# Performance work log

Measured on AMD Instinct MI355X. Metric: run time of the kernel, lower is better.

Reference implementation:

```python
import jax, jax.numpy as jnp
import numpy as np

B, N, DIM = 16, 1024, 512
H, DH = 8, 64  # heads, dim_head; inner_dim = H*DH = 512
MASK_VAL = -1e-9  # value ASSIGNED (not added) to diagonal, per original code


def setup_inputs() -> dict:
    key = jax.random.key(0)
    ks = jax.random.split(key, 8)
    w = 0.02  # small init so softmax is not saturated
    x = jax.random.normal(ks[0], (B, N, DIM), dtype=jnp.float32)
    Wq = jax.random.normal(ks[1], (DIM, H * DH), dtype=jnp.float32) * w
    Wkv = jax.random.normal(ks[2], (DIM, 2 * H * DH), dtype=jnp.float32) * w
    scale = jnp.full((H,), DH ** -0.5, dtype=jnp.float32)  # nn.Parameter(scale*ones(heads))
    mix_pre = jax.random.normal(ks[3], (H, H), dtype=jnp.float32) * w
    mix_post = jax.random.normal(ks[4], (H, H), dtype=jnp.float32) * w
    Wout = jax.random.normal(ks[5], (H * DH, DIM), dtype=jnp.float32) * w
    bout = jnp.zeros((DIM,), dtype=jnp.float32)
    return {"x": x, "Wq": Wq, "Wkv": Wkv, "scale": scale,
            "mix_pre": mix_pre, "mix_post": mix_post, "Wout": Wout, "bout": bout}


def reference(x, Wq, Wkv, scale, mix_pre, mix_post, Wout, bout):
    b, n, _ = x.shape
    # projections -> [b, h, n, d]
    q = (x @ Wq).reshape(b, n, H, DH).transpose(0, 2, 1, 3)
    kv = (x @ Wkv).reshape(b, n, 2, H, DH)
    k = kv[:, :, 0].transpose(0, 2, 1, 3)
    v = kv[:, :, 1].transpose(0, 2, 1, 3)
    # LMSA: per-head learned scale
    dots = jnp.einsum('bhid,bhjd->bhij', q, k) * scale[None, :, None, None]
    # if_patch_attn: set diagonal entries to -1e-9 (assignment, as in torch)
    eye = jnp.eye(n, dtype=bool)
    dots = jnp.where(eye, jnp.float32(MASK_VAL), dots)
    # talking heads: pre-softmax head mix
    dots = jnp.einsum('bhij,hg->bgij', dots, mix_pre)
    attn = jax.nn.softmax(dots, axis=-1)
    # post-softmax head mix
    attn = jnp.einsum('bhij,hg->bgij', attn, mix_post)
    out = jnp.einsum('bhij,bhjd->bhid', attn, v)  # [b,h,n,d]
    out = out.transpose(0, 2, 1, 3).reshape(b, n, H * DH)
    return out @ Wout + bout
```

## Files before the change

kernel.cpp:

```cpp
#include <hip/hip_runtime.h>
#include <math.h>


typedef short bf16x8 __attribute__((ext_vector_type(8)));
typedef float f32x4 __attribute__((ext_vector_type(4)));

__device__ __forceinline__ f32x4 mfma16(bf16x8 a, bf16x8 b, f32x4 c) {
  return __builtin_amdgcn_mfma_f32_16x16x32_bf16(a, b, c, 0, 0, 0);
}

__device__ __forceinline__ unsigned short f2bf(float f) {
  unsigned u = __float_as_uint(f);
  u = (u + 0x7fffu + ((u >> 16) & 1u)) >> 16;
  return (unsigned short)u;
}

__device__ __forceinline__ void splitbf(float f, unsigned short& hi,
                                        unsigned short& lo) {
  hi = f2bf(f);
  float fh = __uint_as_float((unsigned)hi << 16);
  lo = f2bf(f - fh);
}

__device__ __forceinline__ f32x4 zero4() {
  f32x4 z = {0.f, 0.f, 0.f, 0.f};
  return z;
}

namespace {

constexpr int kB = 16, kN = 1024, kH = 8;

__global__ __launch_bounds__(256) void prep(
    const float* __restrict__ Wq, const float* __restrict__ Wkv,
    const float* __restrict__ Wout, unsigned short* __restrict__ WTh,
    unsigned short* __restrict__ WTl, unsigned short* __restrict__ WoTh,
    unsigned short* __restrict__ WoTl) {
  int id = blockIdx.x * 256 + threadIdx.x;
  unsigned short h, l;
  if (id < 1536 * 512) {
    int n = id >> 9, k = id & 511;
    float v = (n < 512) ? Wq[(size_t)k * 512 + n]
                        : Wkv[(size_t)k * 1024 + (n - 512)];
    splitbf(v, h, l);
    WTh[id] = h; WTl[id] = l;
  } else {
    int id2 = id - 1536 * 512;
    int n = id2 >> 9, k = id2 & 511;
    splitbf(Wout[(size_t)k * 512 + n], h, l);
    WoTh[id2] = h; WoTl[id2] = l;
  }
}

__global__ __launch_bounds__(256) void gemm_qkv(
    const float* __restrict__ X, const unsigned short* __restrict__ WTh,
    const unsigned short* __restrict__ WTl, const float* __restrict__ scale,
    unsigned short* __restrict__ Qh, unsigned short* __restrict__ Ql,
    unsigned short* __restrict__ Kh, unsigned short* __restrict__ Kl,
    unsigned short* __restrict__ Vh, unsigned short* __restrict__ Vl) {
  __shared__ unsigned short Ah[128 * 72], Al[128 * 72];
  __shared__ unsigned short Bh[128 * 72], Bl[128 * 72];
  const int tid = threadIdx.x;
  const int n0 = blockIdx.x * 128, m0 = blockIdx.y * 128;
  const int w = tid >> 6, lane = tid & 63, quad = lane >> 4, ln = lane & 15;
  const int mw = (w >> 1) * 64, nw = (w & 1) * 64;
  const int srow = tid >> 3, schk = (tid & 7) * 8;
  f32x4 acc[4][4];
#pragma unroll
  for (int i = 0; i < 4; ++i)
#pragma unroll
    for (int j = 0; j < 4; ++j) acc[i][j] = zero4();
  for (int k0 = 0; k0 < 512; k0 += 64) {
    float xa[4][8];
    uint4 bh4[4], bl4[4];
#pragma unroll
    for (int c2 = 0; c2 < 4; ++c2) {
      const float* xs = X + (size_t)(m0 + c2 * 32 + srow) * 512 + k0 + schk;
      *(float4*)&xa[c2][0] = *(const float4*)xs;
      *(float4*)&xa[c2][4] = *(const float4*)(xs + 4);
      size_t boff = (size_t)(n0 + c2 * 32 + srow) * 512 + k0 + schk;
      bh4[c2] = *(const uint4*)(WTh + boff);
      bl4[c2] = *(const uint4*)(WTl + boff);
    }
    __syncthreads();
#pragma unroll
    for (int c2 = 0; c2 < 4; ++c2) {
      unsigned short hh[8], ll[8];
#pragma unroll
      for (int e = 0; e < 8; ++e) splitbf(xa[c2][e], hh[e], ll[e]);
      uint4 ph, pl;
      ph.x = hh[0] | ((unsigned)hh[1] << 16); pl.x = ll[0] | ((unsigned)ll[1] << 16);
      ph.y = hh[2] | ((unsigned)hh[3] << 16); pl.y = ll[2] | ((unsigned)ll[3] << 16);
      ph.z = hh[4] | ((unsigned)hh[5] << 16); pl.z = ll[4] | ((unsigned)ll[5] << 16);
      ph.w = hh[6] | ((unsigned)hh[7] << 16); pl.w = ll[6] | ((unsigned)ll[7] << 16);
      *(uint4*)&Ah[(c2 * 32 + srow) * 72 + schk] = ph;
      *(uint4*)&Al[(c2 * 32 + srow) * 72 + schk] = pl;
      *(uint4*)&Bh[(c2 * 32 + srow) * 72 + schk] = bh4[c2];
      *(uint4*)&Bl[(c2 * 32 + srow) * 72 + schk] = bl4[c2];
    }
    __syncthreads();
#pragma unroll
    for (int ks = 0; ks < 2; ++ks) {
      bf16x8 afh[4], afl[4], bfh[4], bfl[4];
#pragma unroll
      for (int t = 0; t < 4; ++t) {
        int ao = (mw + t * 16 + ln) * 72 + ks * 32 + quad * 8;
        int bo = (nw + t * 16 + ln) * 72 + ks * 32 + quad * 8;
        afh[t] = *(const bf16x8*)&Ah[ao];
        afl[t] = *(const bf16x8*)&Al[ao];
        bfh[t] = *(const bf16x8*)&Bh[bo];
        bfl[t] = *(const bf16x8*)&Bl[bo];
      }
#pragma unroll
      for (int mt = 0; mt < 4; ++mt)
#pragma unroll
        for (int nt = 0; nt < 4; ++nt) {
          acc[mt][nt] = mfma16(afh[mt], bfh[nt], acc[mt][nt]);
          acc[mt][nt] = mfma16(afh[mt], bfl[nt], acc[mt][nt]);
          acc[mt][nt] = mfma16(afl[mt], bfh[nt], acc[mt][nt]);
        }
    }
  }
  const int region = n0 >> 9;
#pragma unroll
  for (int nt = 0; nt < 4; ++nt) {
    const int col = n0 + nw + nt * 16 + ln;
    const int local = col - region * 512;
    const int hh = local >> 6, d = local & 63;
    const float sc = (region == 0) ? scale[hh] : 1.f;
#pragma unroll
    for (int mt = 0; mt < 4; ++mt) {
#pragma unroll
      for (int r = 0; r < 4; ++r) {
        const int row = m0 + mw + mt * 16 + quad * 4 + r;
        const int b = row >> 10, i = row & 1023;
        unsigned short vh, vl;
        splitbf(acc[mt][nt][r] * sc, vh, vl);
        if (region == 0) {
          size_t o = (((size_t)(b * 8 + hh) * 1024 + i) << 6) + d;
          Qh[o] = vh; Ql[o] = vl;
        } else if (region == 1) {
          size_t o = (((size_t)(b * 8 + hh) * 1024 + i) << 6) + d;
          Kh[o] = vh; Kl[o] = vl;
        } else {
          size_t o = (((size_t)(b * 8 + hh) * 64 + d) << 10) + i;
          Vh[o] = vh; Vl[o] = vl;
        }
      }
    }
  }
}

__global__ __launch_bounds__(256) void attn_lsum(
    const unsigned short* __restrict__ Qh_g, const unsigned short* __restrict__ Ql_g,
    const unsigned short* __restrict__ Kh, const unsigned short* __restrict__ Kl,
    const float* __restrict__ mix_pre, float* __restrict__ IL) {
  __shared__ unsigned short Qsh[128 * 72];
  __shared__ float mixp_s[64], dfix_s[8];
  __shared__ float lred[512];
  const int tid = threadIdx.x;
  const int b = blockIdx.y, ib = blockIdx.x, i0 = ib * 16;
  const int w = tid >> 6, lane = tid & 63, quad = lane >> 4, ln = lane & 15;
  const int jh = w * 16;
  if (tid < 64) mixp_s[tid] = mix_pre[tid];
  if (tid < 8) {
    float s = 0.f;
#pragma unroll
    for (int h = 0; h < 8; ++h) s += mix_pre[h * 8 + tid];
    dfix_s[tid] = -1e-9f * s;
  }
#pragma unroll
  for (int c = 0; c < 4; ++c) {
    int v = tid + 256 * c;
    int row = v >> 3, chk = (v & 7) * 8;
    int h = row >> 4, ii = row & 15;
    *(uint4*)&Qsh[row * 72 + chk] =
        *(const uint4*)(Qh_g + (((size_t)(b * 8 + h) * 1024 + i0 + ii) << 6) + chk);
  }
  __syncthreads();
  const int ig0 = i0 + quad * 4;
  float l[8][4];
#pragma unroll
  for (int a = 0; a < 8; ++a)
#pragma unroll
    for (int r = 0; r < 4; ++r) l[a][r] = 0.f;
  const size_t qoff = (((size_t)(b * 8) * 1024 + i0 + ln) << 6) + quad * 8;
#pragma unroll 1
  for (int j0 = 0; j0 < 1024; j0 += 64) {
    const int jj = j0 + jh + ln;
    bf16x8 kh_r[2][2], kl_r[2][2], ql_r[2][2];
#pragma unroll
    for (int ks = 0; ks < 2; ++ks) {
      size_t kro = (((size_t)(b * 8) * 1024 + jj) << 6) + ks * 32 + quad * 8;
      kh_r[0][ks] = *(const bf16x8*)(Kh + kro);
      kl_r[0][ks] = *(const bf16x8*)(Kl + kro);
      ql_r[0][ks] = *(const bf16x8*)(Ql_g + qoff + ks * 32);
    }
    f32x4 S[8];
    int cur = 0;
#pragma unroll
    for (int h = 0; h < 8; ++h) {
      const int nxt = cur ^ 1;
      if (h < 7) {
#pragma unroll
        for (int ks = 0; ks < 2; ++ks) {
          size_t kro = (((size_t)(b * 8 + h + 1) * 1024 + jj) << 6) + ks * 32 + quad * 8;
          kh_r[nxt][ks] = *(const bf16x8*)(Kh + kro);
          kl_r[nxt][ks] = *(const bf16x8*)(Kl + kro);
          ql_r[nxt][ks] = *(const bf16x8*)(Ql_g + qoff + (size_t)(h + 1) * 65536 + ks * 32);
        }
      }
      f32x4 acc = zero4();
#pragma unroll
      for (int ks = 0; ks < 2; ++ks) {
        bf16x8 ah = *(const bf16x8*)&Qsh[(h * 16 + ln) * 72 + ks * 32 + quad * 8];
        acc = mfma16(ah, kh_r[cur][ks], acc);
        acc = mfma16(ah, kl_r[cur][ks], acc);
        acc = mfma16(ql_r[cur][ks], kh_r[cur][ks], acc);
      }
      S[h] = acc;
      cur = nxt;
    }
    const int dr = jj - ig0;
#pragma unroll
    for (int a = 0; a < 8; ++a) {
      f32x4 sm = S[0] * mixp_s[a];
#pragma unroll
      for (int h = 1; h < 8; ++h) sm += S[h] * mixp_s[h * 8 + a];
      const float df = dfix_s[a];
#pragma unroll
      for (int r = 0; r < 4; ++r) {
        float vv = (r == dr) ? df : sm[r];
        l[a][r] += __expf(vv);
      }
    }
  }
#pragma unroll
  for (int off = 1; off < 16; off <<= 1)
#pragma unroll
    for (int a = 0; a < 8; ++a)
#pragma unroll
      for (int r = 0; r < 4; ++r) l[a][r] += __shfl_xor(l[a][r], off);
  if (ln == 0) {
#pragma unroll
    for (int a = 0; a < 8; ++a)
#pragma unroll
      for (int r = 0; r < 4; ++r)
        lred[(w * 8 + a) * 16 + quad * 4 + r] = l[a][r];
  }
  __syncthreads();
  if (tid < 128) {
    int a = tid >> 4, i = tid & 15;
    float s = lred[a * 16 + i] + lred[(8 + a) * 16 + i] +
              lred[(16 + a) * 16 + i] + lred[(24 + a) * 16 + i];
    IL[(((size_t)b * 8 + a) << 10) + i0 + i] = 1.f / s;
  }
}

__global__ __launch_bounds__(256) void attn_pv(
    const unsigned short* __restrict__ Qh_g, const unsigned short* __restrict__ Ql_g,
    const unsigned short* __restrict__ Kh, const unsigned short* __restrict__ Kl,
    const unsigned short* __restrict__ Vh, const unsigned short* __restrict__ Vl,
    const float* __restrict__ IL, const float* __restrict__ mix_pre,
    const float* __restrict__ mix_post, float* __restrict__ OA) {
  __shared__ unsigned short Qsh[128 * 72];
  __shared__ unsigned short Wsh[128 * 72], Wsl[128 * 72];
  __shared__ float mixp_s[64], mixq_s[64], dfix_s[8];
  __shared__ float Ils[8][16];
  const int tid = threadIdx.x;
  const int b = blockIdx.y, ib = blockIdx.x, i0 = ib * 16;
  const int w = tid >> 6, lane = tid & 63, quad = lane >> 4, ln = lane & 15;
  const int jh = w * 16;
  if (tid < 64) { mixp_s[tid] = mix_pre[tid]; mixq_s[tid] = mix_post[tid]; }
  if (tid < 8) {
    float s = 0.f;
#pragma unroll
    for (int h = 0; h < 8; ++h) s += mix_pre[h * 8 + tid];
    dfix_s[tid] = -1e-9f * s;
  }
  if (tid >= 128) {
    int a = (tid - 128) >> 4, i = tid & 15;
    Ils[a][i] = IL[(((size_t)b * 8 + a) << 10) + i0 + i];
  }
#pragma unroll
  for (int c = 0; c < 4; ++c) {
    int v = tid + 256 * c;
    int row = v >> 3, chk = (v & 7) * 8;
    int h = row >> 4, ii = row & 15;
    *(uint4*)&Qsh[row * 72 + chk] =
        *(const uint4*)(Qh_g + (((size_t)(b * 8 + h) * 1024 + i0 + ii) << 6) + chk);
  }
  __syncthreads();
  const int ig0 = i0 + quad * 4;
  const int cw = w * 2;
  const size_t qoff = (((size_t)(b * 8) * 1024 + i0 + ln) << 6) + quad * 8;
  f32x4 O[2][4];
#pragma unroll
  for (int cc = 0; cc < 2; ++cc)
#pragma unroll
    for (int nt = 0; nt < 4; ++nt) O[cc][nt] = zero4();
  bf16x8 vbh[2][4], vbl[2][4];
#pragma unroll
  for (int nt = 0; nt < 4; ++nt) {
    size_t vo = (((size_t)(b * 8 + cw) * 64 + nt * 16 + ln) << 10) + quad * 8;
    vbh[0][nt] = *(const bf16x8*)(Vh + vo);
    vbl[0][nt] = *(const bf16x8*)(Vl + vo);
  }
#pragma unroll 1
  for (int j0 = 0; j0 < 1024; j0 += 64) {
    const int jj = j0 + jh + ln;
    bf16x8 kh_r[2][2], kl_r[2][2], ql_r[2][2];
#pragma unroll
    for (int ks = 0; ks < 2; ++ks) {
      size_t kro = (((size_t)(b * 8) * 1024 + jj) << 6) + ks * 32 + quad * 8;
      kh_r[0][ks] = *(const bf16x8*)(Kh + kro);
      kl_r[0][ks] = *(const bf16x8*)(Kl + kro);
      ql_r[0][ks] = *(const bf16x8*)(Ql_g + qoff + ks * 32);
    }
    f32x4 S[8];
    int cur = 0;
#pragma unroll
    for (int h = 0; h < 8; ++h) {
      const int nxt = cur ^ 1;
      if (h < 7) {
#pragma unroll
        for (int ks = 0; ks < 2; ++ks) {
          size_t kro = (((size_t)(b * 8 + h + 1) * 1024 + jj) << 6) + ks * 32 + quad * 8;
          kh_r[nxt][ks] = *(const bf16x8*)(Kh + kro);
          kl_r[nxt][ks] = *(const bf16x8*)(Kl + kro);
          ql_r[nxt][ks] = *(const bf16x8*)(Ql_g + qoff + (size_t)(h + 1) * 65536 + ks * 32);
        }
      }
      f32x4 acc = zero4();
#pragma unroll
      for (int ks = 0; ks < 2; ++ks) {
        bf16x8 ah = *(const bf16x8*)&Qsh[(h * 16 + ln) * 72 + ks * 32 + quad * 8];
        acc = mfma16(ah, kh_r[cur][ks], acc);
        acc = mfma16(ah, kl_r[cur][ks], acc);
        acc = mfma16(ql_r[cur][ks], kh_r[cur][ks], acc);
      }
      S[h] = acc;
      cur = nxt;
    }
    const int dr = jj - ig0;
    f32x4 P[8];
#pragma unroll
    for (int a = 0; a < 8; ++a) {
      f32x4 sm = S[0] * mixp_s[a];
#pragma unroll
      for (int h = 1; h < 8; ++h) sm += S[h] * mixp_s[h * 8 + a];
      const float df = dfix_s[a];
      f32x4 il4 = *(const f32x4*)&Ils[a][quad * 4];
      f32x4 p;
#pragma unroll
      for (int r = 0; r < 4; ++r) {
        float vv = (r == dr) ? df : sm[r];
        p[r] = __expf(vv) * il4[r];
      }
      P[a] = p;
    }
#pragma unroll
    for (int c = 0; c < 8; ++c) {
      f32x4 wv = P[0] * mixq_s[c];
#pragma unroll
      for (int a = 1; a < 8; ++a) wv += P[a] * mixq_s[a * 8 + c];
#pragma unroll
      for (int r = 0; r < 4; ++r) {
        unsigned short vhh, vll;
        splitbf(wv[r], vhh, vll);
        int o = (c * 16 + quad * 4 + r) * 72 + jh + ln;
        Wsh[o] = vhh; Wsl[o] = vll;
      }
    }
    __syncthreads();
#pragma unroll
    for (int s = 0; s < 4; ++s) {
      const int cc = s >> 1, ks = s & 1;
      const int c = cw + cc;
      const int vcur = s & 1, vnxt = vcur ^ 1;
      if (s < 3) {
        const int cc2 = (s + 1) >> 1, ks2 = (s + 1) & 1;
#pragma unroll
        for (int nt = 0; nt < 4; ++nt) {
          size_t vo = (((size_t)(b * 8 + cw + cc2) * 64 + nt * 16 + ln) << 10) +
                      j0 + ks2 * 32 + quad * 8;
          vbh[vnxt][nt] = *(const bf16x8*)(Vh + vo);
          vbl[vnxt][nt] = *(const bf16x8*)(Vl + vo);
        }
      } else if (j0 < 960) {
#pragma unroll
        for (int nt = 0; nt < 4; ++nt) {
          size_t vo = (((size_t)(b * 8 + cw) * 64 + nt * 16 + ln) << 10) +
                      j0 + 64 + quad * 8;
          vbh[vnxt][nt] = *(const bf16x8*)(Vh + vo);
          vbl[vnxt][nt] = *(const bf16x8*)(Vl + vo);
        }
      }
      bf16x8 a_h = *(const bf16x8*)&Wsh[(c * 16 + ln) * 72 + ks * 32 + quad * 8];
      bf16x8 a_l = *(const bf16x8*)&Wsl[(c * 16 + ln) * 72 + ks * 32 + quad * 8];
#pragma unroll
      for (int nt = 0; nt < 4; ++nt) {
        O[cc][nt] = mfma16(a_h, vbh[vcur][nt], O[cc][nt]);
        O[cc][nt] = mfma16(a_h, vbl[vcur][nt], O[cc][nt]);
        O[cc][nt] = mfma16(a_l, vbh[vcur][nt], O[cc][nt]);
      }
    }
    __syncthreads();
  }
#pragma unroll
  for (int cc = 0; cc < 2; ++cc)
#pragma unroll
    for (int nt = 0; nt < 4; ++nt)
#pragma unroll
      for (int r = 0; r < 4; ++r) {
        const int i = i0 + quad * 4 + r;
        const int col = (cw + cc) * 64 + nt * 16 + ln;
        OA[((size_t)(b * 1024 + i) << 9) + col] = O[cc][nt][r];
      }
}

__global__ __launch_bounds__(256) void gemm_out(
    const float* __restrict__ A, const unsigned short* __restrict__ BTh,
    const unsigned short* __restrict__ BTl, const float* __restrict__ bias,
    float* __restrict__ Out) {
  __shared__ unsigned short Ah[128 * 72], Al[128 * 72];
  __shared__ unsigned short Bh[128 * 72], Bl[128 * 72];
  const int tid = threadIdx.x;
  const int n0 = blockIdx.x * 128, m0 = blockIdx.y * 128;
  const int w = tid >> 6, lane = tid & 63, quad = lane >> 4, ln = lane & 15;
  const int mw = (w >> 1) * 64, nw = (w & 1) * 64;
  const int srow = tid >> 3, schk = (tid & 7) * 8;
  f32x4 acc[4][4];
#pragma unroll
  for (int i = 0; i < 4; ++i)
#pragma unroll
    for (int j = 0; j < 4; ++j) acc[i][j] = zero4();
  for (int k0 = 0; k0 < 512; k0 += 64) {
    float xa[4][8];
    uint4 bh4[4], bl4[4];
#pragma unroll
    for (int c2 = 0; c2 < 4; ++c2) {
      const float* xs = A + (size_t)(m0 + c2 * 32 + srow) * 512 + k0 + schk;
      *(float4*)&xa[c2][0] = *(const float4*)xs;
      *(float4*)&xa[c2][4] = *(const float4*)(xs + 4);
      size_t boff = (size_t)(n0 + c2 * 32 + srow) * 512 + k0 + schk;
      bh4[c2] = *(const uint4*)(BTh + boff);
      bl4[c2] = *(const uint4*)(BTl + boff);
    }
    __syncthreads();
#pragma unroll
    for (int c2 = 0; c2 < 4; ++c2) {
      unsigned short hh[8], ll[8];
#pragma unroll
      for (int e = 0; e < 8; ++e) splitbf(xa[c2][e], hh[e], ll[e]);
      uint4 ph, pl;
      ph.x = hh[0] | ((unsigned)hh[1] << 16); pl.x = ll[0] | ((unsigned)ll[1] << 16);
      ph.y = hh[2] | ((unsigned)hh[3] << 16); pl.y = ll[2] | ((unsigned)ll[3] << 16);
      ph.z = hh[4] | ((unsigned)hh[5] << 16); pl.z = ll[4] | ((unsigned)ll[5] << 16);
      ph.w = hh[6] | ((unsigned)hh[7] << 16); pl.w = ll[6] | ((unsigned)ll[7] << 16);
      *(uint4*)&Ah[(c2 * 32 + srow) * 72 + schk] = ph;
      *(uint4*)&Al[(c2 * 32 + srow) * 72 + schk] = pl;
      *(uint4*)&Bh[(c2 * 32 + srow) * 72 + schk] = bh4[c2];
      *(uint4*)&Bl[(c2 * 32 + srow) * 72 + schk] = bl4[c2];
    }
    __syncthreads();
#pragma unroll
    for (int ks = 0; ks < 2; ++ks) {
      bf16x8 afh[4], afl[4], bfh[4], bfl[4];
#pragma unroll
      for (int t = 0; t < 4; ++t) {
        int ao = (mw + t * 16 + ln) * 72 + ks * 32 + quad * 8;
        int bo = (nw + t * 16 + ln) * 72 + ks * 32 + quad * 8;
        afh[t] = *(const bf16x8*)&Ah[ao];
        afl[t] = *(const bf16x8*)&Al[ao];
        bfh[t] = *(const bf16x8*)&Bh[bo];
        bfl[t] = *(const bf16x8*)&Bl[bo];
      }
#pragma unroll
      for (int mt = 0; mt < 4; ++mt)
#pragma unroll
        for (int nt = 0; nt < 4; ++nt) {
          acc[mt][nt] = mfma16(afh[mt], bfh[nt], acc[mt][nt]);
          acc[mt][nt] = mfma16(afh[mt], bfl[nt], acc[mt][nt]);
          acc[mt][nt] = mfma16(afl[mt], bfh[nt], acc[mt][nt]);
        }
    }
  }
#pragma unroll
  for (int nt = 0; nt < 4; ++nt) {
    const int col = n0 + nw + nt * 16 + ln;
    const float bcol = bias[col];
#pragma unroll
    for (int mt = 0; mt < 4; ++mt) {
#pragma unroll
      for (int r = 0; r < 4; ++r) {
        const int row = m0 + mw + mt * 16 + quad * 4 + r;
        Out[(size_t)row * 512 + col] = acc[mt][nt][r] + bcol;
      }
    }
  }
}

}

extern "C" void kernel_launch(void* const* d_in, const int* in_sizes, int n_in,
                              void* d_out, int out_size, void* d_ws, size_t ws_size,
                              hipStream_t stream) {
  const float* x        = (const float*)d_in[0];
  const float* Wq       = (const float*)d_in[1];
  const float* Wkv      = (const float*)d_in[2];
  const float* scale    = (const float*)d_in[3];
  const float* mix_pre  = (const float*)d_in[4];
  const float* mix_post = (const float*)d_in[5];
  const float* Wout     = (const float*)d_in[6];
  const float* bout     = (const float*)d_in[7];
  float* out = (float*)d_out;

  char* p = (char*)d_ws;
  const size_t qsz = (size_t)kB * kH * kN * 64;
  unsigned short* WTh  = (unsigned short*)p; p += (size_t)1536 * 512 * 2;
  unsigned short* WTl  = (unsigned short*)p; p += (size_t)1536 * 512 * 2;
  unsigned short* WoTh = (unsigned short*)p; p += (size_t)512 * 512 * 2;
  unsigned short* WoTl = (unsigned short*)p; p += (size_t)512 * 512 * 2;
  unsigned short* Qh   = (unsigned short*)p; p += qsz * 2;
  unsigned short* Ql   = (unsigned short*)p; p += qsz * 2;
  unsigned short* Kh   = (unsigned short*)p; p += qsz * 2;
  unsigned short* Kl   = (unsigned short*)p; p += qsz * 2;
  unsigned short* Vh   = (unsigned short*)p; p += qsz * 2;
  unsigned short* Vl   = (unsigned short*)p; p += qsz * 2;
  float* OA = (float*)p; p += (size_t)kB * kN * 512 * 4;
  float* ILp = (float*)p; p += (size_t)131072 * 4;

  prep<<<4096, 256, 0, stream>>>(Wq, Wkv, Wout, WTh, WTl, WoTh, WoTl);
  gemm_qkv<<<dim3(12, 128), 256, 0, stream>>>(x, WTh, WTl, scale,
                                              Qh, Ql, Kh, Kl, Vh, Vl);
  attn_lsum<<<dim3(64, 16), 256, 0, stream>>>(Qh, Ql, Kh, Kl, mix_pre, ILp);
  attn_pv<<<dim3(64, 16), 256, 0, stream>>>(Qh, Ql, Kh, Kl, Vh, Vl, ILp,
                                            mix_pre, mix_post, OA);
  gemm_out<<<dim3(4, 128), 256, 0, stream>>>(OA, WoTh, WoTl, bout, out);
}
```

Baseline: 1.579 ms.

## Stage V transpose through LDS and drop Q-low term in lse pass

The QKV GEMM epilogue now transposes the V tile through shared memory so V is written as packed 16-byte stores instead of scattered 2-byte stores along the strided i dimension. Separately, the log-sum-exp pass drops the Ql*Kh correction MFMA and the Ql global loads, using only the Qh*(Kh+Kl) split product. This lowers epilogue store traffic and cuts the lse kernel's MFMA and load work by about a third, at the cost of slightly lower precision in the softmax normaliser, which may no longer exactly match the numerator computed in attn_pv.

```diff
diff --git a/kernel.cpp b/kernel.cpp
--- a/kernel.cpp
+++ b/kernel.cpp
@@ -58,8 +58,11 @@
     unsigned short* __restrict__ Qh, unsigned short* __restrict__ Ql,
     unsigned short* __restrict__ Kh, unsigned short* __restrict__ Kl,
     unsigned short* __restrict__ Vh, unsigned short* __restrict__ Vl) {
-  __shared__ unsigned short Ah[128 * 72], Al[128 * 72];
-  __shared__ unsigned short Bh[128 * 72], Bl[128 * 72];
+  __shared__ __align__(16) char gblob[4 * 128 * 72 * 2];
+  unsigned short* Ah = (unsigned short*)gblob;
+  unsigned short* Al = Ah + 128 * 72;
+  unsigned short* Bh = Al + 128 * 72;
+  unsigned short* Bl = Bh + 128 * 72;
   const int tid = threadIdx.x;
   const int n0 = blockIdx.x * 128, m0 = blockIdx.y * 128;
   const int w = tid >> 6, lane = tid & 63, quad = lane >> 4, ln = lane & 15;
@@ -122,37 +125,75 @@
     }
   }
   const int region = n0 >> 9;
-#pragma unroll
-  for (int nt = 0; nt < 4; ++nt) {
-    const int col = n0 + nw + nt * 16 + ln;
-    const int local = col - region * 512;
-    const int hh = local >> 6, d = local & 63;
-    const float sc = (region == 0) ? scale[hh] : 1.f;
-#pragma unroll
-    for (int mt = 0; mt < 4; ++mt) {
-#pragma unroll
-      for (int r = 0; r < 4; ++r) {
-        const int row = m0 + mw + mt * 16 + quad * 4 + r;
-        const int b = row >> 10, i = row & 1023;
-        unsigned short vh, vl;
-        splitbf(acc[mt][nt][r] * sc, vh, vl);
-        if (region == 0) {
+  if (region < 2) {
+#pragma unroll
+    for (int nt = 0; nt < 4; ++nt) {
+      const int col = n0 + nw + nt * 16 + ln;
+      const int local = col - region * 512;
+      const int hh = local >> 6, d = local & 63;
+      const float sc = (region == 0) ? scale[hh] : 1.f;
+#pragma unroll
+      for (int mt = 0; mt < 4; ++mt) {
+#pragma unroll
+        for (int r = 0; r < 4; ++r) {
+          const int row = m0 + mw + mt * 16 + quad * 4 + r;
+          const int b = row >> 10, i = row & 1023;
+          unsigned short vh, vl;
+          splitbf(acc[mt][nt][r] * sc, vh, vl);
           size_t o = (((size_t)(b * 8 + hh) * 1024 + i) << 6) + d;
-          Qh[o] = vh; Ql[o] = vl;
-        } else if (region == 1) {
-          size_t o = (((size_t)(b * 8 + hh) * 1024 + i) << 6) + d;
-          Kh[o] = vh; Kl[o] = vl;
-        } else {
-          size_t o = (((size_t)(b * 8 + hh) * 64 + d) << 10) + i;
-          Vh[o] = vh; Vl[o] = vl;
-        }
-      }
+          if (region == 0) { Qh[o] = vh; Ql[o] = vl; }
+          else             { Kh[o] = vh; Kl[o] = vl; }
+        }
+      }
+    }
+  } else {
+    __syncthreads();
+    unsigned short* Th = (unsigned short*)gblob;
+    unsigned short* Tl = Th + 128 * 132;
+#pragma unroll
+    for (int nt = 0; nt < 4; ++nt) {
+      const int coll = nw + nt * 16 + ln;
+#pragma unroll
+      for (int mt = 0; mt < 4; ++mt) {
+#pragma unroll
+        for (int r = 0; r < 4; ++r) {
+          const int mrow = mw + mt * 16 + quad * 4 + r;
+          unsigned short vh, vl;
+          splitbf(acc[mt][nt][r], vh, vl);
+          Th[mrow * 132 + coll] = vh;
+          Tl[mrow * 132 + coll] = vl;
+        }
+      }
+    }
+    __syncthreads();
+    const int b = m0 >> 10, ibase = m0 & 1023;
+#pragma unroll
+    for (int k = 0; k < 8; ++k) {
+      const int chunk = tid + 256 * k;
+      const int coll = chunk >> 4;
+      const int ii8 = (chunk & 15) * 8;
+      const int local512 = (n0 - 1024) + coll;
+      const int hh = local512 >> 6, d = local512 & 63;
+      unsigned short h8[8], l8[8];
+#pragma unroll
+      for (int e = 0; e < 8; ++e) {
+        h8[e] = Th[(ii8 + e) * 132 + coll];
+        l8[e] = Tl[(ii8 + e) * 132 + coll];
+      }
+      uint4 ph, pl;
+      ph.x = h8[0] | ((unsigned)h8[1] << 16); pl.x = l8[0] | ((unsigned)l8[1] << 16);
+      ph.y = h8[2] | ((unsigned)h8[3] << 16); pl.y = l8[2] | ((unsigned)l8[3] << 16);
+      ph.z = h8[4] | ((unsigned)h8[5] << 16); pl.z = l8[4] | ((unsigned)l8[5] << 16);
+      ph.w = h8[6] | ((unsigned)h8[7] << 16); pl.w = l8[6] | ((unsigned)l8[7] << 16);
+      size_t o = (((size_t)(b * 8 + hh) * 64 + d) << 10) + ibase + ii8;
+      *(uint4*)(Vh + o) = ph;
+      *(uint4*)(Vl + o) = pl;
     }
   }
 }
 
 __global__ __launch_bounds__(256) void attn_lsum(
-    const unsigned short* __restrict__ Qh_g, const unsigned short* __restrict__ Ql_g,
+    const unsigned short* __restrict__ Qh_g,
     const unsigned short* __restrict__ Kh, const unsigned short* __restrict__ Kl,
     const float* __restrict__ mix_pre, float* __restrict__ IL) {
   __shared__ unsigned short Qsh[128 * 72];
@@ -184,17 +225,15 @@
   for (int a = 0; a < 8; ++a)
 #pragma unroll
     for (int r = 0; r < 4; ++r) l[a][r] = 0.f;
-  const size_t qoff = (((size_t)(b * 8) * 1024 + i0 + ln) << 6) + quad * 8;
 #pragma unroll 1
   for (int j0 = 0; j0 < 1024; j0 += 64) {
     const int jj = j0 + jh + ln;
-    bf16x8 kh_r[2][2], kl_r[2][2], ql_r[2][2];
+    bf16x8 kh_r[2][2], kl_r[2][2];
 #pragma unroll
     for (int ks = 0; ks < 2; ++ks) {
       size_t kro = (((size_t)(b * 8) * 1024 + jj) << 6) + ks * 32 + quad * 8;
       kh_r[0][ks] = *(const bf16x8*)(Kh + kro);
       kl_r[0][ks] = *(const bf16x8*)(Kl + kro);
-      ql_r[0][ks] = *(const bf16x8*)(Ql_g + qoff + ks * 32);
     }
     f32x4 S[8];
     int cur = 0;
@@ -207,7 +246,6 @@
           size_t kro = (((size_t)(b * 8 + h + 1) * 1024 + jj) << 6) + ks * 32 + quad * 8;
           kh_r[nxt][ks] = *(const bf16x8*)(Kh + kro);
           kl_r[nxt][ks] = *(const bf16x8*)(Kl + kro);
-          ql_r[nxt][ks] = *(const bf16x8*)(Ql_g + qoff + (size_t)(h + 1) * 65536 + ks * 32);
         }
       }
       f32x4 acc = zero4();
@@ -216,7 +254,6 @@
         bf16x8 ah = *(const bf16x8*)&Qsh[(h * 16 + ln) * 72 + ks * 32 + quad * 8];
         acc = mfma16(ah, kh_r[cur][ks], acc);
         acc = mfma16(ah, kl_r[cur][ks], acc);
-        acc = mfma16(ql_r[cur][ks], kh_r[cur][ks], acc);
       }
       S[h] = acc;
       cur = nxt;
@@ -534,7 +571,7 @@
   prep<<<4096, 256, 0, stream>>>(Wq, Wkv, Wout, WTh, WTl, WoTh, WoTl);
   gemm_qkv<<<dim3(12, 128), 256, 0, stream>>>(x, WTh, WTl, scale,
                                               Qh, Ql, Kh, Kl, Vh, Vl);
-  attn_lsum<<<dim3(64, 16), 256, 0, stream>>>(Qh, Ql, Kh, Kl, mix_pre, ILp);
+  attn_lsum<<<dim3(64, 16), 256, 0, stream>>>(Qh, Kh, Kl, mix_pre, ILp);
   attn_pv<<<dim3(64, 16), 256, 0, stream>>>(Qh, Ql, Kh, Kl, Vh, Vl, ILp,
                                             mix_pre, mix_post, OA);
   gemm_out<<<dim3(4, 128), 256, 0, stream>>>(OA, WoTh, WoTl, bout, out);
```

After: 1.508 ms. 4.5% less time.
